# Optimization experiments

Measured on AMD Instinct MI355X. Metric: run time of the kernel, lower is better.

The kernel has to match this reference:

```python
import jax, jax.numpy as jnp
import numpy as np

# dims matching init_kwargs
B, N, D = 2, 4096, 1024
H, LH = 16, 8
GH = H - LH            # global (FAVOR+) heads
DH = D // H            # 64 per-head dim
M = 256                # performer random features
W = 256                # local attention window
EPS = 1e-4


def softmax_kernel(data, proj, is_query):
    """FAVOR+ positive softmax kernel features. data: [b,h,n,d], proj: [m,d]."""
    dn = data.shape[-1] ** -0.25                       # data_normalizer
    ratio = proj.shape[0] ** -0.5
    data_dash = jnp.einsum('bhnd,md->bhnm', data * dn, proj)
    diag = jnp.sum(data ** 2, axis=-1, keepdims=True) * 0.5 * dn ** 2
    if is_query:
        stab = jnp.max(data_dash, axis=-1, keepdims=True)
    else:
        stab = jnp.max(data_dash)
    return ratio * (jnp.exp(data_dash - diag - stab) + EPS)


def linear_attention(q, k, v):
    """Non-causal performer attention. q,k: [b,h,n,m], v: [b,h,n,d]."""
    k_sum = k.sum(axis=-2)                                        # [b,h,m]
    d_inv = 1.0 / jnp.einsum('bhnm,bhm->bhn', q, k_sum)
    ctx = jnp.einsum('bhnm,bhnd->bhmd', k, v)                     # [b,h,m,d]
    return jnp.einsum('bhnm,bhmd,bhn->bhnd', q, ctx, d_inv)


def local_attention(q, k, v, w):
    """Windowed attention: each window of w queries attends to windows i-1,i,i+1."""
    b, h, n, d = q.shape
    nw = n // w
    scale = d ** -0.5
    qw = q.reshape(b, h, nw, w, d)
    kw = k.reshape(b, h, nw, w, d)
    vw = v.reshape(b, h, nw, w, d)
    kp = jnp.pad(kw, ((0, 0), (0, 0), (1, 1), (0, 0), (0, 0)))
    vp = jnp.pad(vw, ((0, 0), (0, 0), (1, 1), (0, 0), (0, 0)))
    kk = jnp.concatenate([kp[:, :, :-2], kp[:, :, 1:-1], kp[:, :, 2:]], axis=3)  # [b,h,nw,3w,d]
    vv = jnp.concatenate([vp[:, :, :-2], vp[:, :, 1:-1], vp[:, :, 2:]], axis=3)
    wi = jnp.arange(nw)
    back_ok = jnp.broadcast_to((wi > 0)[:, None], (nw, w))
    mid_ok = jnp.ones((nw, w), dtype=bool)
    fwd_ok = jnp.broadcast_to((wi < nw - 1)[:, None], (nw, w))
    valid = jnp.concatenate([back_ok, mid_ok, fwd_ok], axis=-1)   # [nw, 3w]
    scores = jnp.einsum('bhiqd,bhikd->bhiqk', qw, kk) * scale
    scores = jnp.where(valid[None, None, :, None, :], scores, -1e9)
    attn = jax.nn.softmax(scores, axis=-1)
    out = jnp.einsum('bhiqk,bhikd->bhiqd', attn, vv)
    return out.reshape(b, h, n, d)


def _orthogonal_projection(m, d, seed=0):
    """Gaussian orthogonal random matrix (scaling=0) as in performer FeatureMap."""
    rng = np.random.default_rng(seed)
    blocks = []
    for _ in range(m // d):
        a = rng.standard_normal((d, d))
        qmat, _ = np.linalg.qr(a)
        blocks.append(qmat.T)
    un = np.concatenate(blocks, axis=0)                # [m, d] orthonormal rows per block
    mult = np.linalg.norm(rng.standard_normal((m, d)), axis=1, keepdims=True)
    return jnp.asarray(mult * un, dtype=jnp.float32)


def setup_inputs() -> dict:
    key = jax.random.key(0)
    k1, k2, k3, k4, k5, k6 = jax.random.split(key, 6)
    s = 0.02
    return {
        'x': jax.random.normal(k1, (B, N, D), dtype=jnp.float32),
        'Wq': jax.random.normal(k2, (D, D), dtype=jnp.float32) * s,
        'Wk': jax.random.normal(k3, (D, D), dtype=jnp.float32) * s,
        'Wv': jax.random.normal(k4, (D, D), dtype=jnp.float32) * s,
        'Wo': jax.random.normal(k5, (D, D), dtype=jnp.float32) * s,
        'bo': jax.random.normal(k6, (D,), dtype=jnp.float32) * s,
        'proj': _orthogonal_projection(M, DH),
    }


def reference(x, Wq, Wk, Wv, Wo, bo, proj):
    b, n, _ = x.shape
    # qkv projections (weights stored [in,out]; no qkv bias)
    q = (x @ Wq).reshape(b, n, H, DH).transpose(0, 2, 1, 3)
    k = (x @ Wk).reshape(b, n, H, DH).transpose(0, 2, 1, 3)
    v = (x @ Wv).reshape(b, n, H, DH).transpose(0, 2, 1, 3)
    # split global / local heads
    qg, ql = q[:, :GH], q[:, GH:]
    kg, kl = k[:, :GH], k[:, GH:]
    vg, vl = v[:, :GH], v[:, GH:]
    # global FAVOR+ path
    phi_q = softmax_kernel(qg, proj, is_query=True)
    phi_k = softmax_kernel(kg, proj, is_query=False)
    out_g = linear_attention(phi_q, phi_k, vg)
    # local windowed path
    out_l = local_attention(ql, kl, vl, W)
    out = jnp.concatenate([out_g, out_l], axis=1)          # [b,H,n,DH]
    out = out.transpose(0, 2, 1, 3).reshape(b, n, H * DH)
    return out @ Wo + bo
```

## Files before the change

### kernel.cpp

```cpp
#include <hip/hip_runtime.h>
#include <hip/hip_bf16.h>

#define B_ 2
#define N_ 4096
#define D_ 1024
#define QLD_ 3072
#define H_ 16
#define GH_ 8
#define DH_ 64
#define M_ 256
#define W_ 256
#define NW_ 16
#define EPS_ 1e-4f
#define RATIO_ 0.0625f
#define R_ (B_*N_)

typedef __attribute__((ext_vector_type(8))) short short8;
typedef __attribute__((ext_vector_type(4))) short short4_;
typedef __attribute__((ext_vector_type(4))) float float4_;

__device__ __forceinline__ float b2f(unsigned short u){
  union { unsigned int i; float f; } x; x.i = ((unsigned int)u) << 16; return x.f;
}
__device__ __forceinline__ unsigned short f2b(float f){
  unsigned int u = __float_as_uint(f);
  u = u + 0x7FFFu + ((u >> 16) & 1u);
  return (unsigned short)(u >> 16);
}
__device__ __forceinline__ void gl_lds16(const unsigned short* g, unsigned short* l){
  __builtin_amdgcn_global_load_lds((const __attribute__((address_space(1))) unsigned int*)g,
                                   (__attribute__((address_space(3))) unsigned int*)l, 16, 0, 0);
}

__global__ void cast_f32_bf16(const float* __restrict__ src, unsigned short* __restrict__ dst,
                              const float* __restrict__ proj, unsigned short* __restrict__ projb,
                              int n8){
  int i = blockIdx.x*256 + threadIdx.x;
  if (i < M_*DH_) projb[i] = f2b(proj[i]*0.35355339059327373f);
  if (i >= n8) return;
  const float4_* sp = (const float4_*)src + (size_t)i*2;
  float4_ a = sp[0], b = sp[1];
  short8 o;
  o[0]=(short)f2b(a[0]); o[1]=(short)f2b(a[1]); o[2]=(short)f2b(a[2]); o[3]=(short)f2b(a[3]);
  o[4]=(short)f2b(b[0]); o[5]=(short)f2b(b[1]); o[6]=(short)f2b(b[2]); o[7]=(short)f2b(b[3]);
  *((short8*)dst + i) = o;
}

__global__ void transpose_w(const float* w0, const float* w1, const float* w2, const float* w3,
                            unsigned short* t0, unsigned short* t1, unsigned short* t2, unsigned short* t3){
  const float* src; unsigned short* dst;
  switch (blockIdx.z){
    case 0: src = w0; dst = t0; break;
    case 1: src = w1; dst = t1; break;
    case 2: src = w2; dst = t2; break;
    default: src = w3; dst = t3; break;
  }
  __shared__ float tile[64][65];
  int r0 = blockIdx.x*64, c0 = blockIdx.y*64;
  for (int it = 0; it < 16; ++it){
    int idx = it*256 + threadIdx.x;
    int r = idx >> 6, c = idx & 63;
    tile[r][c] = src[(size_t)(r0 + r)*D_ + c0 + c];
  }
  __syncthreads();
  for (int it = 0; it < 16; ++it){
    int idx = it*256 + threadIdx.x;
    int r = idx >> 6, c = idx & 63;
    dst[(size_t)(c0 + r)*D_ + r0 + c] = f2b(tile[c][r]);
  }
}

__global__ void transpose_v(const unsigned short* __restrict__ Vb, unsigned short* __restrict__ Vt,
                            float* __restrict__ vcol){
  __shared__ unsigned short tile[64*72];
  int nt = blockIdx.x, h = blockIdx.y, b = blockIdx.z;
  int n0 = nt*64, col0 = h*64;
  int tid = threadIdx.x;
  int r = tid >> 2, c16 = (tid & 3)*16;
  #pragma unroll
  for (int g = 0; g < 2; ++g){
    short8 v = *(const short8*)&Vb[((size_t)b*N_ + n0 + r)*QLD_ + col0 + c16 + g*8];
    #pragma unroll
    for (int e = 0; e < 8; ++e) tile[r*72 + c16 + g*8 + e] = (unsigned short)v[e];
  }
  __syncthreads();
  if (h < GH_){
    int c = tid & 63, g = tid >> 6;
    float s = 0.f;
    #pragma unroll
    for (int i = 0; i < 16; ++i) s += b2f(tile[(g*16 + i)*72 + c]);
    atomicAdd(&vcol[(b*GH_ + h)*64 + c], s);
  }
  int d = tid >> 2, ng = (tid & 3)*16;
  short8 o0, o1;
  #pragma unroll
  for (int e = 0; e < 8; ++e){ o0[e] = (short)tile[(ng + e)*72 + d]; o1[e] = (short)tile[(ng + 8 + e)*72 + d]; }
  size_t ob = ((size_t)(b*H_ + h)*64 + d)*N_ + n0 + ng;
  *(short8*)&Vt[ob] = o0;
  *(short8*)&Vt[ob + 8] = o1;
}

template<int FINAL>
__launch_bounds__(256)
__global__ void gemm_bf16(const unsigned short* __restrict__ A, const unsigned short* __restrict__ Bt,
                          unsigned short* __restrict__ Cb, float* __restrict__ Cf,
                          const float* __restrict__ bias, int K, int Ncols){
  __shared__ __attribute__((aligned(16))) unsigned short As0[128*32];
  __shared__ __attribute__((aligned(16))) unsigned short Bs0[128*32];
  __shared__ __attribute__((aligned(16))) unsigned short As1[128*32];
  __shared__ __attribute__((aligned(16))) unsigned short Bs1[128*32];
  int tid = threadIdx.x, lane = tid & 63, wave = tid >> 6;
  int bm = blockIdx.x*128, bn = blockIdx.y*128;
  int wm = (wave >> 1)*64, wn = (wave & 1)*64;
  float4_ acc[4][4];
  #pragma unroll
  for (int i = 0; i < 4; ++i)
    #pragma unroll
    for (int j = 0; j < 4; ++j)
      #pragma unroll
      for (int r = 0; r < 4; ++r) acc[i][j][r] = 0.f;
  int srow = tid >> 2, c = tid & 3;
  int scol = (c ^ ((srow >> 1) & 3))*8;
  const unsigned short* a0 = &A[(size_t)(bm + srow)*K + scol];
  const unsigned short* a1 = &A[(size_t)(bm + 64 + srow)*K + scol];
  const unsigned short* b0 = &Bt[(size_t)(bn + srow)*K + scol];
  const unsigned short* b1 = &Bt[(size_t)(bn + 64 + srow)*K + scol];
  int p4 = lane >> 4, l15 = lane & 15;
  for (int k0 = 0; k0 < K; k0 += 64){
    gl_lds16(a0,      &As0[tid*8]);
    gl_lds16(a1,      &As0[2048 + tid*8]);
    gl_lds16(b0,      &Bs0[tid*8]);
    gl_lds16(b1,      &Bs0[2048 + tid*8]);
    gl_lds16(a0 + 32, &As1[tid*8]);
    gl_lds16(a1 + 32, &As1[2048 + tid*8]);
    gl_lds16(b0 + 32, &Bs1[tid*8]);
    gl_lds16(b1 + 32, &Bs1[2048 + tid*8]);
    a0 += 64; a1 += 64; b0 += 64; b1 += 64;
    __syncthreads();
    short8 af[4], bf[4];
    #pragma unroll
    for (int i = 0; i < 4; ++i){
      int row = wm + i*16 + l15;
      af[i] = *(const short8*)&As0[row*32 + (p4 ^ ((row >> 1) & 3))*8];
    }
    #pragma unroll
    for (int j = 0; j < 4; ++j){
      int row = wn + j*16 + l15;
      bf[j] = *(const short8*)&Bs0[row*32 + (p4 ^ ((row >> 1) & 3))*8];
    }
    #pragma unroll
    for (int i = 0; i < 4; ++i)
      #pragma unroll
      for (int j = 0; j < 4; ++j)
        acc[i][j] = __builtin_amdgcn_mfma_f32_16x16x32_bf16(af[i], bf[j], acc[i][j], 0, 0, 0);
    #pragma unroll
    for (int i = 0; i < 4; ++i){
      int row = wm + i*16 + l15;
      af[i] = *(const short8*)&As1[row*32 + (p4 ^ ((row >> 1) & 3))*8];
    }
    #pragma unroll
    for (int j = 0; j < 4; ++j){
      int row = wn + j*16 + l15;
      bf[j] = *(const short8*)&Bs1[row*32 + (p4 ^ ((row >> 1) & 3))*8];
    }
    #pragma unroll
    for (int i = 0; i < 4; ++i)
      #pragma unroll
      for (int j = 0; j < 4; ++j)
        acc[i][j] = __builtin_amdgcn_mfma_f32_16x16x32_bf16(af[i], bf[j], acc[i][j], 0, 0, 0);
    __syncthreads();
  }
  int rr = p4*4, cc = l15;
  #pragma unroll
  for (int i = 0; i < 4; ++i)
    #pragma unroll
    for (int j = 0; j < 4; ++j)
      #pragma unroll
      for (int r = 0; r < 4; ++r){
        size_t row = bm + wm + i*16 + rr + r;
        int col = bn + wn + j*16 + cc;
        if (FINAL) Cf[row*(size_t)Ncols + col] = acc[i][j][r] + bias[col];
        else       Cb[row*(size_t)Ncols + col] = f2b(acc[i][j][r]);
      }
}

__launch_bounds__(256)
__global__ void phik_finish(const unsigned short* __restrict__ Kb, const unsigned short* __restrict__ projb,
                            unsigned short* __restrict__ phikT, float* __restrict__ ksum,
                            float* __restrict__ blkmax){
  __shared__ __attribute__((aligned(16))) unsigned short pl[256*64];
  __shared__ float sm4[4];
  int tid = threadIdx.x, lane = tid & 63, wave = tid >> 6;
  int h = blockIdx.y, b = blockIdx.z, nb = blockIdx.x;
  int n0 = nb*64;
  int col0 = h*64;
  int kk = (lane >> 4)*8, l15 = lane & 15;
  int bh = b*GH_ + h;
  size_t rowbase = (size_t)b*N_ + n0 + wave*16;
  short8 qa[2];
  #pragma unroll
  for (int ks = 0; ks < 2; ++ks)
    qa[ks] = *(const short8*)&Kb[(rowbase + l15)*QLD_ + col0 + ks*32 + kk];
  short8 pf[4][2];
  #pragma unroll
  for (int i = 0; i < 4; ++i){
    pf[i][0] = *(const short8*)&projb[(size_t)(i*16 + l15)*DH_ + kk];
    pf[i][1] = *(const short8*)&projb[(size_t)(i*16 + l15)*DH_ + 32 + kk];
  }
  float s = 0.f;
  #pragma unroll
  for (int ks = 0; ks < 2; ++ks)
    #pragma unroll
    for (int j = 0; j < 8; ++j){ float q = b2f((unsigned short)qa[ks][j]); s += q*q; }
  s += __shfl_xor(s, 16, 64);
  s += __shfl_xor(s, 32, 64);
  s *= 0.0625f;
  float dg[4];
  #pragma unroll
  for (int r = 0; r < 4; ++r) dg[r] = __shfl(s, (lane & 48) | ((lane >> 4)*4 + r), 64);
  float mxall = -3e38f;
  #pragma unroll
  for (int mt = 0; mt < 16; ++mt){
    short8 c0 = pf[mt & 3][0], c1 = pf[mt & 3][1];
    if (mt < 12){
      pf[mt & 3][0] = *(const short8*)&projb[(size_t)((mt + 4)*16 + l15)*DH_ + kk];
      pf[mt & 3][1] = *(const short8*)&projb[(size_t)((mt + 4)*16 + l15)*DH_ + 32 + kk];
    }
    float4_ a; a[0]=a[1]=a[2]=a[3]=0.f;
    a = __builtin_amdgcn_mfma_f32_16x16x32_bf16(qa[0], c0, a, 0, 0, 0);
    a = __builtin_amdgcn_mfma_f32_16x16x32_bf16(qa[1], c1, a, 0, 0, 0);
    int m = mt*16 + l15;
    #pragma unroll
    for (int r = 0; r < 4; ++r){
      float ddv = a[r];
      mxall = fmaxf(mxall, ddv);
      float v = __expf(ddv - dg[r]);
      int n = wave*16 + (lane>>4)*4 + r;
      int slot = (n >> 3) ^ (m & 7);
      pl[m*64 + slot*8 + (n & 7)] = f2b(v);
    }
  }
  #pragma unroll
  for (int mm = 1; mm < 64; mm <<= 1) mxall = fmaxf(mxall, __shfl_xor(mxall, mm, 64));
  if (lane == 0) sm4[wave] = mxall;
  __syncthreads();
  if (tid == 0)
    blkmax[((size_t)b*GH_ + h)*64 + nb] = fmaxf(fmaxf(sm4[0], sm4[1]), fmaxf(sm4[2], sm4[3]));
  {
    int m = tid;
    float ssum = 0.f;
    #pragma unroll
    for (int j = 0; j < 8; ++j){
      int slot = j ^ (m & 7);
      short8 v = *(const short8*)&pl[m*64 + slot*8];
      #pragma unroll
      for (int e = 0; e < 8; ++e) ssum += b2f((unsigned short)v[e]);
    }
    atomicAdd(&ksum[bh*M_ + m], ssum);
  }
  size_t outb = ((size_t)bh*64 + nb)*256*64;
  int j2 = tid & 7, mlo = tid >> 3;
  #pragma unroll
  for (int s2 = 0; s2 < 8; ++s2){
    int m2 = s2*32 + mlo;
    short8 v = *(const short8*)&pl[m2*64 + (j2 ^ (m2 & 7))*8];
    *(short8*)&phikT[outb + (size_t)m2*64 + j2*8] = v;
  }
}

__launch_bounds__(256)
__global__ void ctx_kernel(const unsigned short* __restrict__ phikT, const unsigned short* __restrict__ Vt,
                           float* __restrict__ ctxp){
  int tid = threadIdx.x, lane = tid & 63, wave = tid >> 6;
  int split = blockIdx.x, h = blockIdx.y, b = blockIdx.z;
  int bh = b*GH_ + h;
  int kk = (lane >> 4)*8, l15 = lane & 15;
  float4_ acc[4][4];
  #pragma unroll
  for (int i = 0; i < 4; ++i)
    #pragma unroll
    for (int j = 0; j < 4; ++j)
      #pragma unroll
      for (int r = 0; r < 4; ++r) acc[i][j][r] = 0.f;
  const unsigned short* Abase = phikT + (size_t)bh*64*256*64;
  const unsigned short* Bbase = Vt + (size_t)(b*H_ + h)*64*N_;
  int n0 = split*256;
  #pragma unroll
  for (int ks = 0; ks < 8; ++ks){
    int n = n0 + ks*32;
    int nb = n >> 6, in0 = n & 32;
    short8 af[4], bf[4];
    #pragma unroll
    for (int mt = 0; mt < 4; ++mt)
      af[mt] = *(const short8*)&Abase[((size_t)nb*256 + wave*64 + mt*16 + l15)*64 + in0 + kk];
    #pragma unroll
    for (int dt = 0; dt < 4; ++dt)
      bf[dt] = *(const short8*)&Bbase[(size_t)(dt*16 + l15)*N_ + n + kk];
    #pragma unroll
    for (int mt = 0; mt < 4; ++mt)
      #pragma unroll
      for (int dt = 0; dt < 4; ++dt)
        acc[mt][dt] = __builtin_amdgcn_mfma_f32_16x16x32_bf16(af[mt], bf[dt], acc[mt][dt], 0, 0, 0);
  }
  int rr = (lane >> 4)*4;
  float* obase = ctxp + (((size_t)split*16 + bh)*256)*64;
  #pragma unroll
  for (int mt = 0; mt < 4; ++mt)
    #pragma unroll
    for (int dt = 0; dt < 4; ++dt)
      #pragma unroll
      for (int r = 0; r < 4; ++r)
        obase[(size_t)(wave*64 + mt*16 + rr + r)*64 + dt*16 + l15] = acc[mt][dt][r];
}

__launch_bounds__(256)
__global__ void ctx_reduce(const float* __restrict__ ctxp, const float* __restrict__ vcol,
                           const float* __restrict__ blkmax, unsigned short* __restrict__ ctxbT){
  __shared__ float tile[16*65];
  __shared__ float smax[4];
  int mt = blockIdx.x, bh = blockIdx.y;
  int tid = threadIdx.x, lane = tid & 63, wave = tid >> 6;
  float bm = -3e38f;
  #pragma unroll
  for (int i = 0; i < 4; ++i) bm = fmaxf(bm, blkmax[i*256 + tid]);
  #pragma unroll
  for (int mm = 1; mm < 64; mm <<= 1) bm = fmaxf(bm, __shfl_xor(bm, mm, 64));
  if (lane == 0) smax[wave] = bm;
  __syncthreads();
  float stab = fmaxf(fmaxf(smax[0], smax[1]), fmaxf(smax[2], smax[3]));
  float es = RATIO_*__expf(-stab);
  float epsr = RATIO_*EPS_;
  int ml = tid >> 4, d4 = (tid & 15)*4;
  const float* base = ctxp + ((size_t)bh*256 + mt*16 + ml)*64 + d4;
  float4_ acc; acc[0]=acc[1]=acc[2]=acc[3]=0.f;
  #pragma unroll
  for (int sp = 0; sp < 16; ++sp){
    float4_ v = *(const float4_*)(base + (size_t)sp*16*256*64);
    acc[0] += v[0]; acc[1] += v[1]; acc[2] += v[2]; acc[3] += v[3];
  }
  #pragma unroll
  for (int e = 0; e < 4; ++e) acc[e] = es*acc[e] + epsr*vcol[bh*64 + d4 + e];
  *(float4_*)&tile[ml*65 + d4] = acc;
  __syncthreads();
  int d = tid >> 2, mg = (tid & 3)*4;
  short4_ o;
  #pragma unroll
  for (int e = 0; e < 4; ++e) o[e] = (short)f2b(tile[(mg + e)*65 + d]);
  *(short4_*)&ctxbT[((size_t)bh*64 + d)*256 + mt*16 + mg] = o;
}

__launch_bounds__(256)
__global__ void phiq_outg(const unsigned short* __restrict__ Qb, const unsigned short* __restrict__ projb,
                          const unsigned short* __restrict__ ctxbT, const float* __restrict__ ksum_u,
                          const float* __restrict__ blkmax, unsigned short* __restrict__ attnb){
  __shared__ __attribute__((aligned(16))) unsigned short pl[4][16*256];
  __shared__ float ks_l[256];
  __shared__ float smax[4];
  int tid = threadIdx.x, lane = tid & 63, wave = tid >> 6;
  int h = blockIdx.y, b = blockIdx.z;
  int n0 = blockIdx.x*64;
  int col0 = h*64;
  int bh = b*GH_ + h;
  int p4 = lane >> 4, l15 = lane & 15, kk = p4*8;
  {
    float bm = -3e38f;
    #pragma unroll
    for (int i = 0; i < 4; ++i) bm = fmaxf(bm, blkmax[i*256 + tid]);
    #pragma unroll
    for (int mm = 1; mm < 64; mm <<= 1) bm = fmaxf(bm, __shfl_xor(bm, mm, 64));
    if (lane == 0) smax[wave] = bm;
  }
  __syncthreads();
  {
    float stab = fmaxf(fmaxf(smax[0], smax[1]), fmaxf(smax[2], smax[3]));
    float es = __expf(-stab);
    ks_l[tid] = RATIO_*(es*ksum_u[bh*M_ + tid] + EPS_*(float)N_);
  }
  __syncthreads();
  size_t rowbase = (size_t)b*N_ + n0 + wave*16;
  short8 qa[2];
  #pragma unroll
  for (int ks = 0; ks < 2; ++ks)
    qa[ks] = *(const short8*)&Qb[(rowbase + l15)*QLD_ + col0 + ks*32 + kk];
  short8 pf[4][2];
  #pragma unroll
  for (int i = 0; i < 4; ++i){
    pf[i][0] = *(const short8*)&projb[(size_t)(i*16 + l15)*DH_ + kk];
    pf[i][1] = *(const short8*)&projb[(size_t)(i*16 + l15)*DH_ + 32 + kk];
  }
  float s = 0.f;
  #pragma unroll
  for (int ks = 0; ks < 2; ++ks)
    #pragma unroll
    for (int j = 0; j < 8; ++j){ float q = b2f((unsigned short)qa[ks][j]); s += q*q; }
  s += __shfl_xor(s, 16, 64);
  s += __shfl_xor(s, 32, 64);
  s *= 0.0625f;
  float dg[4];
  #pragma unroll
  for (int r = 0; r < 4; ++r) dg[r] = __shfl(s, (lane & 48) | (p4*4 + r), 64);
  float4_ dd[16];
  #pragma unroll
  for (int mt = 0; mt < 16; ++mt){
    short8 c0 = pf[mt & 3][0], c1 = pf[mt & 3][1];
    if (mt < 12){
      pf[mt & 3][0] = *(const short8*)&projb[(size_t)((mt + 4)*16 + l15)*DH_ + kk];
      pf[mt & 3][1] = *(const short8*)&projb[(size_t)((mt + 4)*16 + l15)*DH_ + 32 + kk];
    }
    float4_ a; a[0]=a[1]=a[2]=a[3]=0.f;
    a = __builtin_amdgcn_mfma_f32_16x16x32_bf16(qa[0], c0, a, 0, 0, 0);
    a = __builtin_amdgcn_mfma_f32_16x16x32_bf16(qa[1], c1, a, 0, 0, 0);
    dd[mt] = a;
  }
  unsigned short* plw = &pl[wave][0];
  float dinv[4];
  #pragma unroll
  for (int r = 0; r < 4; ++r){
    float mx = dd[0][r];
    #pragma unroll
    for (int mt = 1; mt < 16; ++mt) mx = fmaxf(mx, dd[mt][r]);
    mx = fmaxf(mx, __shfl_xor(mx, 1, 64));
    mx = fmaxf(mx, __shfl_xor(mx, 2, 64));
    mx = fmaxf(mx, __shfl_xor(mx, 4, 64));
    mx = fmaxf(mx, __shfl_xor(mx, 8, 64));
    float sb = mx + dg[r];
    int row = p4*4 + r;
    float dpr = 0.f;
    #pragma unroll
    for (int mt = 0; mt < 16; ++mt){
      float v = RATIO_*(__expf(dd[mt][r] - sb) + EPS_);
      dpr += v*ks_l[mt*16 + l15];
      int q = mt*2 + (l15 >> 3);
      plw[row*256 + ((q ^ (row & 7)) << 3) + (l15 & 7)] = f2b(v);
    }
    dpr += __shfl_xor(dpr, 1, 64);
    dpr += __shfl_xor(dpr, 2, 64);
    dpr += __shfl_xor(dpr, 4, 64);
    dpr += __shfl_xor(dpr, 8, 64);
    dinv[r] = 1.f/dpr;
  }
  float4_ acc[4];
  #pragma unroll
  for (int dt = 0; dt < 4; ++dt){ acc[dt][0]=acc[dt][1]=acc[dt][2]=acc[dt][3]=0.f; }
  #pragma unroll
  for (int ks = 0; ks < 8; ++ks){
    int q = ks*4 + p4;
    short8 af = *(const short8*)&plw[l15*256 + ((q ^ (l15 & 7)) << 3)];
    #pragma unroll
    for (int dt = 0; dt < 4; ++dt){
      short8 bf = *(const short8*)&ctxbT[((size_t)bh*64 + dt*16 + l15)*M_ + ks*32 + kk];
      acc[dt] = __builtin_amdgcn_mfma_f32_16x16x32_bf16(af, bf, acc[dt], 0, 0, 0);
    }
  }
  #pragma unroll
  for (int dt = 0; dt < 4; ++dt)
    #pragma unroll
    for (int r = 0; r < 4; ++r){
      int rloc = wave*16 + p4*4 + r;
      attnb[((size_t)b*N_ + n0 + rloc)*D_ + col0 + dt*16 + l15] = f2b(acc[dt][r]*dinv[r]);
    }
}

__launch_bounds__(256)
__global__ void local_attn_kernel(const unsigned short* __restrict__ Qb, const unsigned short* __restrict__ Kb,
                                  const unsigned short* __restrict__ Vt, unsigned short* __restrict__ attnb){
  int tid = threadIdx.x, lane = tid & 63, wv = tid >> 6;
  int wg = blockIdx.x;
  int xcd = wg & 7, k = wg >> 3;
  int pair = xcd*2 + (k >> 5);
  int bx = k & 31;
  int hl = pair & 7, b = pair >> 3;
  int w = bx >> 1;
  int col0 = (GH_ + hl)*64;
  int q0 = bx*128 + wv*32;
  int l15 = lane & 15, p4 = lane >> 4, kk = p4*8;
  int sA = ((l15 >> 2) << 3) + (l15 & 3);
  const unsigned short* Kbase = Kb + (size_t)b*N_*QLD_ + col0;
  const unsigned short* Vrow  = Vt + (size_t)(b*H_ + GH_ + hl)*64*N_;
  short8 qa[2][2];
  #pragma unroll
  for (int qt = 0; qt < 2; ++qt)
    #pragma unroll
    for (int ks = 0; ks < 2; ++ks){
      short8 v = *(const short8*)&Qb[((size_t)b*N_ + q0 + qt*16 + l15)*QLD_ + col0 + ks*32 + kk];
      #pragma unroll
      for (int j = 0; j < 8; ++j) v[j] = (short)f2b(b2f((unsigned short)v[j])*0.125f);
      qa[qt][ks] = v;
    }
  float l_part[2] = {0.f, 0.f};
  float4_ accv[2][4];
  #pragma unroll
  for (int qt = 0; qt < 2; ++qt)
    #pragma unroll
    for (int dt = 0; dt < 4; ++dt){ accv[qt][dt][0]=accv[qt][dt][1]=accv[qt][dt][2]=accv[qt][dt][3]=0.f; }
  int wlo = (w > 0) ? w - 1 : 0;
  int whi = (w < NW_ - 1) ? w + 1 : NW_ - 1;
  for (int wi = wlo; wi <= whi; ++wi){
    #pragma unroll
    for (int c = 0; c < 4; ++c){
      int key0 = wi*W_ + c*64;
      const unsigned short* Kc = Kbase + (size_t)key0*QLD_;
      float4_ s[2][4];
      #pragma unroll
      for (int qt = 0; qt < 2; ++qt)
        #pragma unroll
        for (int kt = 0; kt < 4; ++kt){ s[qt][kt][0]=s[qt][kt][1]=s[qt][kt][2]=s[qt][kt][3]=0.f; }
      #pragma unroll
      for (int ks = 0; ks < 2; ++ks){
        short8 kb0 = *(const short8*)&Kc[(size_t)(sA +  0)*QLD_ + ks*32 + kk];
        short8 kb1 = *(const short8*)&Kc[(size_t)(sA +  4)*QLD_ + ks*32 + kk];
        short8 kb2 = *(const short8*)&Kc[(size_t)(sA + 32)*QLD_ + ks*32 + kk];
        short8 kb3 = *(const short8*)&Kc[(size_t)(sA + 36)*QLD_ + ks*32 + kk];
        #pragma unroll
        for (int qt = 0; qt < 2; ++qt){
          s[qt][0] = __builtin_amdgcn_mfma_f32_16x16x32_bf16(kb0, qa[qt][ks], s[qt][0], 0, 0, 0);
          s[qt][1] = __builtin_amdgcn_mfma_f32_16x16x32_bf16(kb1, qa[qt][ks], s[qt][1], 0, 0, 0);
          s[qt][2] = __builtin_amdgcn_mfma_f32_16x16x32_bf16(kb2, qa[qt][ks], s[qt][2], 0, 0, 0);
          s[qt][3] = __builtin_amdgcn_mfma_f32_16x16x32_bf16(kb3, qa[qt][ks], s[qt][3], 0, 0, 0);
        }
      }
      short8 af[2][2];
      #pragma unroll
      for (int qt = 0; qt < 2; ++qt){
        float p[4][4];
        float rs = 0.f;
        #pragma unroll
        for (int kt = 0; kt < 4; ++kt)
          #pragma unroll
          for (int r = 0; r < 4; ++r){
            p[kt][r] = __expf(s[qt][kt][r]);
            rs += p[kt][r];
          }
        l_part[qt] += rs;
        #pragma unroll
        for (int half = 0; half < 2; ++half){
          short8 a;
          #pragma unroll
          for (int r = 0; r < 4; ++r){
            a[r]     = (short)f2b(p[half*2 + 0][r]);
            a[r + 4] = (short)f2b(p[half*2 + 1][r]);
          }
          af[qt][half] = a;
        }
      }
      #pragma unroll
      for (int ks = 0; ks < 2; ++ks){
        short8 vb0 = *(const short8*)&Vrow[(size_t)( 0 + l15)*N_ + key0 + ks*32 + kk];
        short8 vb1 = *(const short8*)&Vrow[(size_t)(16 + l15)*N_ + key0 + ks*32 + kk];
        short8 vb2 = *(const short8*)&Vrow[(size_t)(32 + l15)*N_ + key0 + ks*32 + kk];
        short8 vb3 = *(const short8*)&Vrow[(size_t)(48 + l15)*N_ + key0 + ks*32 + kk];
        #pragma unroll
        for (int qt = 0; qt < 2; ++qt){
          accv[qt][0] = __builtin_amdgcn_mfma_f32_16x16x32_bf16(af[qt][ks], vb0, accv[qt][0], 0, 0, 0);
          accv[qt][1] = __builtin_amdgcn_mfma_f32_16x16x32_bf16(af[qt][ks], vb1, accv[qt][1], 0, 0, 0);
          accv[qt][2] = __builtin_amdgcn_mfma_f32_16x16x32_bf16(af[qt][ks], vb2, accv[qt][2], 0, 0, 0);
          accv[qt][3] = __builtin_amdgcn_mfma_f32_16x16x32_bf16(af[qt][ks], vb3, accv[qt][3], 0, 0, 0);
        }
      }
    }
  }
  #pragma unroll
  for (int qt = 0; qt < 2; ++qt){
    float lv = l_part[qt];
    lv += __shfl_xor(lv, 16, 64);
    lv += __shfl_xor(lv, 32, 64);
    float ilq[4];
    #pragma unroll
    for (int r = 0; r < 4; ++r)
      ilq[r] = 1.f/__shfl(lv, (lane & 48) | (p4*4 + r), 64);
    #pragma unroll
    for (int dt = 0; dt < 4; ++dt)
      #pragma unroll
      for (int r = 0; r < 4; ++r)
        attnb[((size_t)b*N_ + q0 + qt*16 + p4*4 + r)*D_ + col0 + dt*16 + l15] = f2b(accv[qt][dt][r]*ilq[r]);
  }
}

extern "C" void kernel_launch(void* const* d_in, const int* in_sizes, int n_in,
                              void* d_out, int out_size, void* d_ws, size_t ws_size,
                              hipStream_t stream){
  const float* x    = (const float*)d_in[0];
  const float* Wq   = (const float*)d_in[1];
  const float* Wk   = (const float*)d_in[2];
  const float* Wv   = (const float*)d_in[3];
  const float* Wo   = (const float*)d_in[4];
  const float* bo   = (const float*)d_in[5];
  const float* proj = (const float*)d_in[6];
  float* out = (float*)d_out;
  char* ws = (char*)d_ws;

  const size_t o_Wqt  = 0;
  const size_t o_Wkt  = o_Wqt  + (size_t)D_*D_*2;
  const size_t o_Wvt  = o_Wkt  + (size_t)D_*D_*2;
  const size_t o_Wot  = o_Wvt  + (size_t)D_*D_*2;
  const size_t o_Xb   = o_Wot  + (size_t)D_*D_*2;
  const size_t o_QKV  = o_Xb   + (size_t)R_*D_*2;
  const size_t o_Vt   = o_QKV  + (size_t)R_*QLD_*2;
  const size_t o_phikT= o_Vt   + (size_t)B_*H_*DH_*N_*2;
  const size_t o_ctxp = o_phikT+ (size_t)B_*GH_*N_*M_*2;
  const size_t o_ksum = o_ctxp + (size_t)16*B_*GH_*M_*DH_*4;
  const size_t o_vcol = o_ksum + (size_t)B_*GH_*M_*4;
  const size_t o_ctxT = o_vcol + (size_t)B_*GH_*DH_*4;
  const size_t o_projb= o_ctxT + (size_t)B_*GH_*DH_*M_*2;
  const size_t o_bmax = o_projb+ (size_t)M_*DH_*2;

  unsigned short* Wqt  = (unsigned short*)(ws + o_Wqt);
  unsigned short* Wkt  = (unsigned short*)(ws + o_Wkt);
  unsigned short* Wvt  = (unsigned short*)(ws + o_Wvt);
  unsigned short* Wot  = (unsigned short*)(ws + o_Wot);
  unsigned short* Xb   = (unsigned short*)(ws + o_Xb);
  unsigned short* attnb= Xb;
  unsigned short* QKV  = (unsigned short*)(ws + o_QKV);
  unsigned short* Vt   = (unsigned short*)(ws + o_Vt);
  unsigned short* phikT= (unsigned short*)(ws + o_phikT);
  float*          ctxp = (float*)(ws + o_ctxp);
  float*          ksum = (float*)(ws + o_ksum);
  float*          vcol = (float*)(ws + o_vcol);
  unsigned short* ctxT = (unsigned short*)(ws + o_ctxT);
  unsigned short* projb= (unsigned short*)(ws + o_projb);
  float*          bmax = (float*)(ws + o_bmax);

  (void)in_sizes; (void)n_in; (void)out_size; (void)ws_size;

  (void)hipMemsetAsync(ws + o_ksum, 0, (size_t)B_*GH_*M_*4 + (size_t)B_*GH_*DH_*4, stream);
  cast_f32_bf16<<<R_*D_/8/256, 256, 0, stream>>>(x, Xb, proj, projb, R_*D_/8);
  transpose_w<<<dim3(16,16,4), 256, 0, stream>>>(Wq, Wk, Wv, Wo, Wqt, Wkt, Wvt, Wot);

  gemm_bf16<0><<<dim3(64,24), 256, 0, stream>>>(Xb, Wqt, QKV, nullptr, nullptr, D_, QLD_);

  transpose_v<<<dim3(64,16,2), 256, 0, stream>>>(QKV + 2048, Vt, vcol);

  phik_finish<<<dim3(64,8,2), 256, 0, stream>>>(QKV + 1024, projb, phikT, ksum, bmax);

  ctx_kernel<<<dim3(16,8,2), 256, 0, stream>>>(phikT, Vt, ctxp);
  ctx_reduce<<<dim3(16,16), 256, 0, stream>>>(ctxp, vcol, bmax, ctxT);
  phiq_outg<<<dim3(64,8,2), 256, 0, stream>>>(QKV, projb, ctxT, ksum, bmax, attnb);
  local_attn_kernel<<<512, 256, 0, stream>>>(QKV, QKV + 1024, Vt, attnb);

  gemm_bf16<1><<<dim3(64,8), 256, 0, stream>>>(attnb, Wot, nullptr, out, bo, D_, D_);
}
```

Baseline: 248.7 us.

## Double-buffer LDS tiles in bf16 GEMM to overlap global loads with MFMA

```diff
diff --git a/kernel.cpp b/kernel.cpp
--- a/kernel.cpp
+++ b/kernel.cpp
@@ -105,10 +105,10 @@
 __global__ void gemm_bf16(const unsigned short* __restrict__ A, const unsigned short* __restrict__ Bt,
                           unsigned short* __restrict__ Cb, float* __restrict__ Cf,
                           const float* __restrict__ bias, int K, int Ncols){
-  __shared__ __attribute__((aligned(16))) unsigned short As0[128*32];
-  __shared__ __attribute__((aligned(16))) unsigned short Bs0[128*32];
-  __shared__ __attribute__((aligned(16))) unsigned short As1[128*32];
-  __shared__ __attribute__((aligned(16))) unsigned short Bs1[128*32];
+  __shared__ __attribute__((aligned(16))) unsigned short As0[2][4096];
+  __shared__ __attribute__((aligned(16))) unsigned short Bs0[2][4096];
+  __shared__ __attribute__((aligned(16))) unsigned short As1[2][4096];
+  __shared__ __attribute__((aligned(16))) unsigned short Bs1[2][4096];
   int tid = threadIdx.x, lane = tid & 63, wave = tid >> 6;
   int bm = blockIdx.x*128, bn = blockIdx.y*128;
   int wm = (wave >> 1)*64, wn = (wave & 1)*64;
@@ -126,50 +126,67 @@
   const unsigned short* b0 = &Bt[(size_t)(bn + srow)*K + scol];
   const unsigned short* b1 = &Bt[(size_t)(bn + 64 + srow)*K + scol];
   int p4 = lane >> 4, l15 = lane & 15;
-  for (int k0 = 0; k0 < K; k0 += 64){
-    gl_lds16(a0,      &As0[tid*8]);
-    gl_lds16(a1,      &As0[2048 + tid*8]);
-    gl_lds16(b0,      &Bs0[tid*8]);
-    gl_lds16(b1,      &Bs0[2048 + tid*8]);
-    gl_lds16(a0 + 32, &As1[tid*8]);
-    gl_lds16(a1 + 32, &As1[2048 + tid*8]);
-    gl_lds16(b0 + 32, &Bs1[tid*8]);
-    gl_lds16(b1 + 32, &Bs1[2048 + tid*8]);
-    a0 += 64; a1 += 64; b0 += 64; b1 += 64;
+
+#define STAGE_(bi, ko) do{ \
+    gl_lds16(a0 + (ko),      &As0[bi][tid*8]); \
+    gl_lds16(a1 + (ko),      &As0[bi][2048 + tid*8]); \
+    gl_lds16(b0 + (ko),      &Bs0[bi][tid*8]); \
+    gl_lds16(b1 + (ko),      &Bs0[bi][2048 + tid*8]); \
+    gl_lds16(a0 + (ko) + 32, &As1[bi][tid*8]); \
+    gl_lds16(a1 + (ko) + 32, &As1[bi][2048 + tid*8]); \
+    gl_lds16(b0 + (ko) + 32, &Bs1[bi][tid*8]); \
+    gl_lds16(b1 + (ko) + 32, &Bs1[bi][2048 + tid*8]); \
+  }while(0)
+
+#define COMPUTE_(bi) do{ \
+    short8 af[4], bf[4]; \
+    _Pragma("unroll") \
+    for (int i = 0; i < 4; ++i){ \
+      int row = wm + i*16 + l15; \
+      af[i] = *(const short8*)&As0[bi][row*32 + (p4 ^ ((row >> 1) & 3))*8]; \
+    } \
+    _Pragma("unroll") \
+    for (int j = 0; j < 4; ++j){ \
+      int row = wn + j*16 + l15; \
+      bf[j] = *(const short8*)&Bs0[bi][row*32 + (p4 ^ ((row >> 1) & 3))*8]; \
+    } \
+    _Pragma("unroll") \
+    for (int i = 0; i < 4; ++i) \
+      _Pragma("unroll") \
+      for (int j = 0; j < 4; ++j) \
+        acc[i][j] = __builtin_amdgcn_mfma_f32_16x16x32_bf16(af[i], bf[j], acc[i][j], 0, 0, 0); \
+    _Pragma("unroll") \
+    for (int i = 0; i < 4; ++i){ \
+      int row = wm + i*16 + l15; \
+      af[i] = *(const short8*)&As1[bi][row*32 + (p4 ^ ((row >> 1) & 3))*8]; \
+    } \
+    _Pragma("unroll") \
+    for (int j = 0; j < 4; ++j){ \
+      int row = wn + j*16 + l15; \
+      bf[j] = *(const short8*)&Bs1[bi][row*32 + (p4 ^ ((row >> 1) & 3))*8]; \
+    } \
+    _Pragma("unroll") \
+    for (int i = 0; i < 4; ++i) \
+      _Pragma("unroll") \
+      for (int j = 0; j < 4; ++j) \
+        acc[i][j] = __builtin_amdgcn_mfma_f32_16x16x32_bf16(af[i], bf[j], acc[i][j], 0, 0, 0); \
+  }while(0)
+
+  const int NT = K >> 6;
+  STAGE_(0, 0);
+  __syncthreads();
+  #pragma unroll 1
+  for (int t = 0; t < NT; t += 2){
+    if (t + 1 < NT) STAGE_(1, (t + 1) << 6);
+    COMPUTE_(0);
     __syncthreads();
-    short8 af[4], bf[4];
-    #pragma unroll
-    for (int i = 0; i < 4; ++i){
-      int row = wm + i*16 + l15;
-      af[i] = *(const short8*)&As0[row*32 + (p4 ^ ((row >> 1) & 3))*8];
-    }
-    #pragma unroll
-    for (int j = 0; j < 4; ++j){
-      int row = wn + j*16 + l15;
-      bf[j] = *(const short8*)&Bs0[row*32 + (p4 ^ ((row >> 1) & 3))*8];
-    }
-    #pragma unroll
-    for (int i = 0; i < 4; ++i)
-      #pragma unroll
-      for (int j = 0; j < 4; ++j)
-        acc[i][j] = __builtin_amdgcn_mfma_f32_16x16x32_bf16(af[i], bf[j], acc[i][j], 0, 0, 0);
-    #pragma unroll
-    for (int i = 0; i < 4; ++i){
-      int row = wm + i*16 + l15;
-      af[i] = *(const short8*)&As1[row*32 + (p4 ^ ((row >> 1) & 3))*8];
-    }
-    #pragma unroll
-    for (int j = 0; j < 4; ++j){
-      int row = wn + j*16 + l15;
-      bf[j] = *(const short8*)&Bs1[row*32 + (p4 ^ ((row >> 1) & 3))*8];
-    }
-    #pragma unroll
-    for (int i = 0; i < 4; ++i)
-      #pragma unroll
-      for (int j = 0; j < 4; ++j)
-        acc[i][j] = __builtin_amdgcn_mfma_f32_16x16x32_bf16(af[i], bf[j], acc[i][j], 0, 0, 0);
+    if (t + 2 < NT) STAGE_(0, (t + 2) << 6);
+    COMPUTE_(1);
     __syncthreads();
   }
+#undef STAGE_
+#undef COMPUTE_
+
   int rr = p4*4, cc = l15;
   #pragma unroll
   for (int i = 0; i < 4; ++i)
```

Measured after the change: 247.7 us. No clear change (-0.4%).
